# Kernel tuning notes

Measured on AMD Instinct MI355X. Metric: run time of the kernel, lower is better.

## Reference

```python
import jax, jax.numpy as jnp
import numpy as np

N, D1, D2, BW, B = 8, 1024, 1024, 3, 1024
D = D1 * D2
RES_DENOS = [3.0, 5.0, 17.0, 257.0, 65537.0]  # [2^2-1, 2^2+1, 2^4+1, 2^8+1, 2^16+1]
SPLIT_TEMP = 0.01


def ste_floor(x):
    # forward: floor, backward: identity (matches custom round autograd.Function)
    return x + jax.lax.stop_gradient(jnp.floor(x) - x)


def quantize_weights(U, thres_mean):
    beta, alpha = jnp.max(U), jnp.min(U)
    s = (beta - alpha) / RES_DENOS[0]
    vals_sum = s * ste_floor(U / s)  # level 0
    col = jnp.arange(D)[None, :]
    for idx in range(1, BW):
        s = s / RES_DENOS[idx]
        res_err = U - vals_sum                                   # [N, D]
        order = jnp.argsort(res_err, axis=0)                     # [N, D] int
        sorted_err = jnp.take_along_axis(res_err, order, axis=0) # [N, D]
        delta = sorted_err[1:] - sorted_err[:-1]                 # [N-1, D]
        delta = delta / jnp.max(delta)
        # differentiable split points, one per gap between sorted rows
        sp = jax.nn.sigmoid((jnp.mean(delta, axis=1) - jax.nn.sigmoid(thres_mean)[0]) / SPLIT_TEMP)  # [N-1]
        b = jnp.round(sp)                                        # hard 0/1 boundary (zero grad, like torch branch)
        gid = jnp.concatenate([jnp.zeros((1,), sp.dtype), jnp.cumsum(b)]).astype(jnp.int32)  # [N] group id per row
        counts = jax.ops.segment_sum(jnp.ones((N,), U.dtype), gid, num_segments=N)           # [N]
        sums = jax.ops.segment_sum(sorted_err, gid, num_segments=N)                          # [N, D]
        means = sums / jnp.maximum(counts, 1.0)[:, None]
        # grad_ factor: sp at boundary rows, (1-sp) at interior rows, 1 for the last row
        factors = jnp.where(b == 1.0, sp, 1.0 - sp)              # [N-1], in (0,1)
        logf = jnp.concatenate([jnp.log(factors), jnp.zeros((1,), sp.dtype)])  # [N]
        grad_g = jnp.exp(jax.ops.segment_sum(logf, gid, num_segments=N))       # [N] per-group product
        t = grad_g[gid][:, None] * means[gid]                    # [N, D] group value broadcast to member rows
        # scatter back through the sort permutation (== one-hot transfer matmul)
        grouped = jnp.zeros_like(U).at[order, col].set(t)
        vals_sum = vals_sum + s * ste_floor(grouped / s)
    return vals_sum


def setup_inputs() -> dict:
    key = jax.random.key(0)
    kx, ku = jax.random.split(key)
    x = jax.random.normal(kx, (B, N, D1), dtype=jnp.float32)
    # kaiming_normal_ on (N, D): std = sqrt(2 / fan_in) with fan_in = D
    U = jax.random.normal(ku, (N, D), dtype=jnp.float32) * np.sqrt(2.0 / D).astype(np.float32)
    thres_mean = jnp.array([-0.405], dtype=jnp.float32)
    return {"x": x, "U": U, "thres_mean": thres_mean}


def reference(x, U, thres_mean):
    w = quantize_weights(U, thres_mean).reshape(N, D1, D2)
    return jnp.einsum('bnd,ndl->bnl', x, w)
```

## Files before the change

kernel.cpp:

```cpp
#include <hip/hip_runtime.h>
#include <hip/hip_bf16.h>
#include <stdint.h>

#define DD (1 << 20)
#define NPART 4096

typedef float v4f __attribute__((ext_vector_type(4)));
typedef __bf16 bf16x8 __attribute__((ext_vector_type(8)));

struct Scalars {
  float s;
  int   uniform;
  int   done;
  float coef[8];
  float cnti[8];
  int   isend[8];
};

struct Partial {
  double g[7];
  double mx;
};

static __device__ __forceinline__ unsigned short f2bf(float v) {
  unsigned u = __float_as_uint(v);
  u += 0x7fffu + ((u >> 16) & 1u);
  return (unsigned short)(u >> 16);
}

__global__ void k_minmax_partial(const float4* __restrict__ U4, float2* __restrict__ part) {
  int tid = threadIdx.x, bid = blockIdx.x;
  float mn = 3.4e38f, mx = -3.4e38f;
#pragma unroll
  for (int j = 0; j < 8; ++j) {
    float4 v = U4[(size_t)(bid * 8 + j) * 256 + tid];
    mn = fminf(mn, fminf(fminf(v.x, v.y), fminf(v.z, v.w)));
    mx = fmaxf(mx, fmaxf(fmaxf(v.x, v.y), fmaxf(v.z, v.w)));
  }
#pragma unroll
  for (int off = 32; off; off >>= 1) {
    mn = fminf(mn, __shfl_down(mn, off, 64));
    mx = fmaxf(mx, __shfl_down(mx, off, 64));
  }
  __shared__ float2 w4[4];
  if ((tid & 63) == 0) w4[tid >> 6] = make_float2(mn, mx);
  __syncthreads();
  if (tid == 0) {
    for (int i = 1; i < 4; ++i) { mn = fminf(mn, w4[i].x); mx = fmaxf(mx, w4[i].y); }
    part[bid] = make_float2(mn, mx);
  }
}

__global__ void k_minmax_final(const float2* __restrict__ part, Scalars* sc0) {
  int tid = threadIdx.x;
  float mn = 3.4e38f, mx = -3.4e38f;
#pragma unroll
  for (int j = 0; j < 4; ++j) {
    float2 p = part[j * 256 + tid];
    mn = fminf(mn, p.x); mx = fmaxf(mx, p.y);
  }
#pragma unroll
  for (int off = 32; off; off >>= 1) {
    mn = fminf(mn, __shfl_down(mn, off, 64));
    mx = fmaxf(mx, __shfl_down(mx, off, 64));
  }
  __shared__ float2 w4[4];
  if ((tid & 63) == 0) w4[tid >> 6] = make_float2(mn, mx);
  __syncthreads();
  if (tid == 0) {
    for (int i = 1; i < 4; ++i) { mn = fminf(mn, w4[i].x); mx = fmaxf(mx, w4[i].y); }
    sc0->s = (mx - mn) / 3.0f;
  }
}

#define CE2(a, b)                                                        \
  { float ra = r[a], rb = r[b]; int oa = ord[a], ob = ord[b];            \
    bool sw = (ra > rb) || (ra == rb && oa > ob);                        \
    r[a] = sw ? rb : ra; r[b] = sw ? ra : rb;                            \
    ord[a] = sw ? ob : oa; ord[b] = sw ? oa : ob; }

#define SORTNET8                                                          \
  CE2(0,1) CE2(2,3) CE2(4,5) CE2(6,7)                                     \
  CE2(0,2) CE2(1,3) CE2(4,6) CE2(5,7)                                     \
  CE2(1,2) CE2(5,6)                                                       \
  CE2(0,4) CE2(1,5) CE2(2,6) CE2(3,7)                                     \
  CE2(2,4) CE2(3,5)                                                       \
  CE2(1,2) CE2(3,4) CE2(5,6)

#define CEV(a, b) { float ra = q[a], rb = q[b]; q[a] = fminf(ra, rb); q[b] = fmaxf(ra, rb); }
#define SORTNET8V                                                         \
  CEV(0,1) CEV(2,3) CEV(4,5) CEV(6,7)                                     \
  CEV(0,2) CEV(1,3) CEV(4,6) CEV(5,7)                                     \
  CEV(1,2) CEV(5,6)                                                       \
  CEV(0,4) CEV(1,5) CEV(2,6) CEV(3,7)                                     \
  CEV(2,4) CEV(3,5)                                                       \
  CEV(1,2) CEV(3,4) CEV(5,6)

static __device__ __forceinline__ void stats_block_reduce(float dl[7], float mx,
                                                          Partial* __restrict__ po) {
#pragma unroll
  for (int off = 32; off; off >>= 1) {
#pragma unroll
    for (int g = 0; g < 7; ++g) dl[g] += __shfl_down(dl[g], off, 64);
    mx = fmaxf(mx, __shfl_down(mx, off, 64));
  }
  __shared__ double wsum[4][7];
  __shared__ float wmax[4];
  int lane = threadIdx.x & 63, wv = threadIdx.x >> 6;
  if (lane == 0) {
#pragma unroll
    for (int g = 0; g < 7; ++g) wsum[wv][g] = (double)dl[g];
    wmax[wv] = mx;
  }
  __syncthreads();
  if (threadIdx.x == 0) {
#pragma unroll
    for (int g = 0; g < 7; ++g)
      po->g[g] = wsum[0][g] + wsum[1][g] + wsum[2][g] + wsum[3][g];
    po->mx = (double)fmaxf(fmaxf(wmax[0], wmax[1]), fmaxf(wmax[2], wmax[3]));
  }
}

__global__ void k_scalars2(const Partial* __restrict__ part, const Scalars* __restrict__ scin,
                           Scalars* __restrict__ scout, Scalars* __restrict__ scnext,
                           const float* __restrict__ thres, float deno, float deno_next,
                           int check_done) {
  if (check_done && scout->done) return;
  int t = threadIdx.x;
  double g[7] = {0, 0, 0, 0, 0, 0, 0};
  double mx = 0.0;
#pragma unroll
  for (int j = 0; j < NPART / 256; ++j) {
    const Partial& p = part[j * 256 + t];
#pragma unroll
    for (int i = 0; i < 7; ++i) g[i] += p.g[i];
    mx = fmax(mx, p.mx);
  }
#pragma unroll
  for (int off = 32; off; off >>= 1) {
#pragma unroll
    for (int i = 0; i < 7; ++i) g[i] += __shfl_down(g[i], off, 64);
    mx = fmax(mx, __shfl_down(mx, off, 64));
  }
  __shared__ double sg[4][8];
  int lane = t & 63, wv = t >> 6;
  if (lane == 0) {
#pragma unroll
    for (int i = 0; i < 7; ++i) sg[wv][i] = g[i];
    sg[wv][7] = mx;
  }
  __syncthreads();
  if (t != 0) return;
#pragma unroll
  for (int i = 0; i < 7; ++i) g[i] = sg[0][i] + sg[1][i] + sg[2][i] + sg[3][i];
  mx = fmax(fmax(sg[0][7], sg[1][7]), fmax(sg[2][7], sg[3][7]));

  float s = scin->s / deno;
  scout->s = s;
  float md = (float)mx;
  float sigT = 1.f / (1.f + expf(-thres[0]));
  float sp[7], bb[7];
  float zmax = -1e30f;
  for (int gg = 0; gg < 7; ++gg) {
    float mean = (float)(g[gg] / ((double)DD * (double)md));
    float z = (mean - sigT) / 0.01f;
    zmax = fmaxf(zmax, z);
    sp[gg] = 1.f / (1.f + expf(-z));
    bb[gg] = rintf(sp[gg]);
  }
  int gid[8]; gid[0] = 0;
  for (int i = 1; i < 8; ++i) gid[i] = gid[i - 1] + (int)bb[i - 1];
  float counts[8] = {0, 0, 0, 0, 0, 0, 0, 0};
  for (int i = 0; i < 8; ++i) counts[gid[i]] += 1.f;
  float lsum[8] = {0, 0, 0, 0, 0, 0, 0, 0};
  for (int i = 0; i < 7; ++i) {
    float f = (bb[i] == 1.f) ? sp[i] : (1.f - sp[i]);
    lsum[gid[i]] += logf(f);
  }
  float gradg[8];
  for (int gg = 0; gg < 8; ++gg) gradg[gg] = expf(lsum[gg]);
  for (int i = 0; i < 8; ++i) {
    scout->coef[i] = gradg[gid[i]];
    scout->cnti[i] = fmaxf(counts[gid[i]], 1.f);
    scout->isend[i] = (i == 7) || (gid[i + 1] != gid[i]);
  }
  int uni = (gid[7] == 0) ? 1 : 0;
  scout->uniform = uni;

  if (scnext) {
    if (uni && zmax < -21.0f) {
      scnext->s = s / deno_next;
      scnext->uniform = 1;
#pragma unroll
      for (int i = 0; i < 8; ++i) {
        scnext->coef[i] = 1.0f;
        scnext->cnti[i] = 8.0f;
        scnext->isend[i] = (i == 7) ? 1 : 0;
      }
      scnext->done = 1;
    } else {
      scnext->done = 0;
    }
  }
}

static __device__ __forceinline__ void update_core(const float u[8], const float vo[8],
                                                   const Scalars* __restrict__ sc,
                                                   float vnew[8]) {
  float s = sc->s;
  float coef[8], cnti[8]; int isend[8];
#pragma unroll
  for (int i = 0; i < 8; ++i) { coef[i] = sc->coef[i]; cnti[i] = sc->cnti[i]; isend[i] = sc->isend[i]; }
  float r[8]; int ord[8];
#pragma unroll
  for (int n = 0; n < 8; ++n) { r[n] = u[n] - vo[n]; ord[n] = n; }
  SORTNET8
  float endsum[8]; float a = 0.f;
#pragma unroll
  for (int i = 0; i < 8; ++i) { a += r[i]; endsum[i] = a; if (isend[i]) a = 0.f; }
  float t[8]; float gsv = 0.f;
#pragma unroll
  for (int i = 7; i >= 0; --i) {
    if (isend[i]) gsv = endsum[i];
    t[i] = coef[i] * (gsv / cnti[i]);
  }
#pragma unroll
  for (int n = 0; n < 8; ++n) {
    float tv = 0.f;
#pragma unroll
    for (int i = 0; i < 8; ++i) tv = (ord[i] == n) ? t[i] : tv;
    vnew[n] = vo[n] + s * floorf(tv / s);
  }
}

static __device__ __forceinline__ float uniform_delta(const float u[8], const float vo[8],
                                                      float coef0, float cnt0, float s) {
  float q[8];
#pragma unroll
  for (int n = 0; n < 8; ++n) q[n] = u[n] - vo[n];
  SORTNET8V
  float a = 0.f;
#pragma unroll
  for (int i = 0; i < 8; ++i) a += q[i];
  float t = coef0 * (a / cnt0);
  return s * floorf(t / s);
}

static __device__ __forceinline__ void apply_update(const float u[8], const float vo[8],
                                                    const Scalars* __restrict__ sc,
                                                    float vnew[8]) {
  if (sc->uniform) {
    float c = uniform_delta(u, vo, sc->coef[0], sc->cnti[0], sc->s);
#pragma unroll
    for (int n = 0; n < 8; ++n) vnew[n] = vo[n] + c;
  } else {
    update_core(u, vo, sc, vnew);
  }
}

__global__ void k_stats0(const float* __restrict__ U, Partial* __restrict__ part,
                         const Scalars* __restrict__ sc0,
                         const float* __restrict__ x, unsigned short* __restrict__ xT) {
  int t = threadIdx.x;
  if (blockIdx.x < NPART) {
    int d = blockIdx.x * 256 + t;
    float s = sc0->s;
    float q[8];
#pragma unroll
    for (int n = 0; n < 8; ++n) {
      float u = U[((size_t)n << 20) + d];
      q[n] = u - s * floorf(u / s);
    }
    SORTNET8V
    float dl[7]; float mx = 0.f;
#pragma unroll
    for (int g = 0; g < 7; ++g) { dl[g] = q[g + 1] - q[g]; mx = fmaxf(mx, dl[g]); }
    stats_block_reduce(dl, mx, &part[blockIdx.x]);
  } else {
    int bid2 = blockIdx.x - NPART;
#pragma unroll
    for (int j = 0; j < 4; ++j) {
      int i = j * (2048 * 256) + bid2 * 256 + t;
      int kq = i & 255;
      int b  = (i >> 8) & 1023;
      int n  = i >> 18;
      float4 v = *(const float4*)(x + ((size_t)(b * 8 + n) << 10) + (kq << 2));
      ushort4 o = make_ushort4(f2bf(v.x), f2bf(v.y), f2bf(v.z), f2bf(v.w));
      *(ushort4*)(xT + (((size_t)(n << 10 | b)) << 10) + (kq << 2)) = o;
    }
  }
}

__global__ void k_stats1(const float* __restrict__ U, Partial* __restrict__ part,
                         const Scalars* __restrict__ sc0, const Scalars* __restrict__ sc1,
                         const Scalars* __restrict__ sc2) {
  if (sc2->done) return;
  int d = blockIdx.x * 256 + threadIdx.x;
  float s0 = sc0->s;
  float u[8], v0[8], v1[8];
#pragma unroll
  for (int n = 0; n < 8; ++n) {
    u[n] = U[((size_t)n << 20) + d];
    v0[n] = s0 * floorf(u[n] / s0);
  }
  apply_update(u, v0, sc1, v1);
  float q[8];
#pragma unroll
  for (int n = 0; n < 8; ++n) q[n] = u[n] - v1[n];
  SORTNET8V
  float dl[7]; float mx = 0.f;
#pragma unroll
  for (int g = 0; g < 7; ++g) { dl[g] = q[g + 1] - q[g]; mx = fmaxf(mx, dl[g]); }
  stats_block_reduce(dl, mx, &part[blockIdx.x]);
}

__global__ void k_final_pack(const float* __restrict__ U,
                             const Scalars* __restrict__ sc0, const Scalars* __restrict__ sc1,
                             const Scalars* __restrict__ sc2, unsigned short* __restrict__ wT) {
  __shared__ unsigned short stile[8][32][34];
  int t = threadIdx.x;
  int k0 = (blockIdx.x >> 5) * 32;
  int l0 = (blockIdx.x & 31) * 32;
  float s0 = sc0->s;
  int kk = t >> 3;
  int lq = t & 7;
  int d0 = (k0 + kk) * 1024 + l0 + lq * 4;
  float4 u4[8];
#pragma unroll
  for (int n = 0; n < 8; ++n) u4[n] = *(const float4*)(U + ((size_t)n << 20) + d0);
#pragma unroll
  for (int j = 0; j < 4; ++j) {
    float u[8], v0[8], v1[8], v2[8];
#pragma unroll
    for (int n = 0; n < 8; ++n) {
      u[n] = ((const float*)&u4[n])[j];
      v0[n] = s0 * floorf(u[n] / s0);
    }
    apply_update(u, v0, sc1, v1);
    apply_update(u, v1, sc2, v2);
#pragma unroll
    for (int n = 0; n < 8; ++n) stile[n][kk][lq * 4 + j] = f2bf(v2[n]);
  }
  __syncthreads();
  int ll = t >> 3, kq = t & 7;
#pragma unroll
  for (int n = 0; n < 8; ++n) {
    ushort4 o;
    o.x = stile[n][kq * 4 + 0][ll];
    o.y = stile[n][kq * 4 + 1][ll];
    o.z = stile[n][kq * 4 + 2][ll];
    o.w = stile[n][kq * 4 + 3][ll];
    *(ushort4*)(wT + ((size_t)n << 20) + (size_t)(l0 + ll) * 1024 + k0 + kq * 4) = o;
  }
}

__global__ __launch_bounds__(256, 2)
void k_gemm(const unsigned short* __restrict__ xT, const unsigned short* __restrict__ wT,
            float* __restrict__ out) {
  __shared__ bf16x8 sA[1024];
  __shared__ bf16x8 sB[1024];
  const int n  = blockIdx.x;
  const int m0 = blockIdx.y * 128;
  const int l0 = blockIdx.z * 128;
  const int tid = threadIdx.x;
  const int lane = tid & 63;
  const int wv = tid >> 6;
  const int wm = (wv & 1) * 64;
  const int wl = (wv >> 1) * 64;
  const unsigned short* A  = xT + ((size_t)n << 20);
  const unsigned short* Bt = wT + ((size_t)n << 20);

  v4f acc[4][4] = {};
  const int quad = lane >> 4;
  const int r16 = lane & 15;

  for (int kt = 0; kt < 1024; kt += 64) {
#pragma unroll
    for (int rr = 0; rr < 4; ++rr) {
      int cb = rr * 4 + wv;
      int c = cb * 64 + lane;
      int row = c >> 3;
      int gc = (c & 7) ^ (row & 7);
      const unsigned short* ga = A  + (size_t)(m0 + row) * 1024 + kt + gc * 8;
      const unsigned short* gb = Bt + (size_t)(l0 + row) * 1024 + kt + gc * 8;
      __builtin_amdgcn_global_load_lds((const __attribute__((address_space(1))) void*)ga,
                                       (__attribute__((address_space(3))) void*)&sA[cb * 64],
                                       16, 0, 0);
      __builtin_amdgcn_global_load_lds((const __attribute__((address_space(1))) void*)gb,
                                       (__attribute__((address_space(3))) void*)&sB[cb * 64],
                                       16, 0, 0);
    }
    asm volatile("s_waitcnt vmcnt(0)" ::: "memory");
    __syncthreads();

#pragma unroll
    for (int ks = 0; ks < 2; ++ks) {
      bf16x8 af[4], bfr[4];
#pragma unroll
      for (int t = 0; t < 4; ++t) {
        int arow = wm + t * 16 + r16;
        af[t] = sA[arow * 8 + ((ks * 4 + quad) ^ (arow & 7))];
        int brow = wl + t * 16 + r16;
        bfr[t] = sB[brow * 8 + ((ks * 4 + quad) ^ (brow & 7))];
      }
#pragma unroll
      for (int tm = 0; tm < 4; ++tm)
#pragma unroll
        for (int tn = 0; tn < 4; ++tn)
          acc[tm][tn] = __builtin_amdgcn_mfma_f32_16x16x32_bf16(af[tm], bfr[tn], acc[tm][tn], 0, 0, 0);
    }
    __syncthreads();
  }

#pragma unroll
  for (int tm = 0; tm < 4; ++tm)
#pragma unroll
    for (int tn = 0; tn < 4; ++tn)
#pragma unroll
      for (int rr = 0; rr < 4; ++rr) {
        int row = m0 + wm + tm * 16 + quad * 4 + rr;
        int col = l0 + wl + tn * 16 + r16;
        out[(size_t)(row * 8 + n) * 1024 + col] = acc[tm][tn][rr];
      }
}

extern "C" void kernel_launch(void* const* d_in, const int* in_sizes, int n_in,
                              void* d_out, int out_size, void* d_ws, size_t ws_size,
                              hipStream_t stream) {
  const float* x = (const float*)d_in[0];
  const float* U = (const float*)d_in[1];
  const float* thres = (const float*)d_in[2];
  float* out = (float*)d_out;

  char* w = (char*)d_ws;
  Scalars* sc = (Scalars*)w;
  float2* mmpart = (float2*)(w + 4096);
  unsigned short* xT = (unsigned short*)(w + 16384);
  unsigned short* wT = xT + ((size_t)8 << 20);
  Partial* part = (Partial*)(w + 16384 + ((size_t)32 << 20));

  k_minmax_partial<<<1024, 256, 0, stream>>>((const float4*)U, mmpart);
  k_minmax_final<<<1, 256, 0, stream>>>(mmpart, &sc[0]);
  k_stats0<<<NPART + 2048, 256, 0, stream>>>(U, part, &sc[0], x, xT);
  k_scalars2<<<1, 256, 0, stream>>>(part, &sc[0], &sc[1], &sc[2], thres, 5.0f, 17.0f, 0);
  k_stats1<<<NPART, 256, 0, stream>>>(U, part, &sc[0], &sc[1], &sc[2]);
  k_scalars2<<<1, 256, 0, stream>>>(part, &sc[1], &sc[2], nullptr, thres, 17.0f, 0.0f, 1);
  k_final_pack<<<1024, 256, 0, stream>>>(U, &sc[0], &sc[1], &sc[2], wT);
  k_gemm<<<dim3(8, 8, 8), 256, 0, stream>>>(xT, wT, out);
}
```

Measured before the change: 165.8 us.

## Fold single-block scalar reductions into consumer kernels and cut launch count

Removes the separate minmax-final and two single-block scalar kernels. Each consumer block now recomputes the scale and the split-point scalars redundantly from the partials into shared memory. The minmax partial pass is merged with the x transpose/pack, and the stats kernels process four columns per thread, which cuts the partial count from 4096 to 1024. The goal is fewer launches and serial single-block gaps, paid for with redundant per-block reduction work over the partial arrays.

```diff
diff --git a/kernel.cpp b/kernel.cpp
--- a/kernel.cpp
+++ b/kernel.cpp
@@ -3,7 +3,6 @@
 #include <stdint.h>
 
 #define DD (1 << 20)
-#define NPART 4096
 
 typedef float v4f __attribute__((ext_vector_type(4)));
 typedef __bf16 bf16x8 __attribute__((ext_vector_type(8)));
@@ -11,7 +10,6 @@
 struct Scalars {
   float s;
   int   uniform;
-  int   done;
   float coef[8];
   float cnti[8];
   int   isend[8];
@@ -26,51 +24,6 @@
   unsigned u = __float_as_uint(v);
   u += 0x7fffu + ((u >> 16) & 1u);
   return (unsigned short)(u >> 16);
-}
-
-__global__ void k_minmax_partial(const float4* __restrict__ U4, float2* __restrict__ part) {
-  int tid = threadIdx.x, bid = blockIdx.x;
-  float mn = 3.4e38f, mx = -3.4e38f;
-#pragma unroll
-  for (int j = 0; j < 8; ++j) {
-    float4 v = U4[(size_t)(bid * 8 + j) * 256 + tid];
-    mn = fminf(mn, fminf(fminf(v.x, v.y), fminf(v.z, v.w)));
-    mx = fmaxf(mx, fmaxf(fmaxf(v.x, v.y), fmaxf(v.z, v.w)));
-  }
-#pragma unroll
-  for (int off = 32; off; off >>= 1) {
-    mn = fminf(mn, __shfl_down(mn, off, 64));
-    mx = fmaxf(mx, __shfl_down(mx, off, 64));
-  }
-  __shared__ float2 w4[4];
-  if ((tid & 63) == 0) w4[tid >> 6] = make_float2(mn, mx);
-  __syncthreads();
-  if (tid == 0) {
-    for (int i = 1; i < 4; ++i) { mn = fminf(mn, w4[i].x); mx = fmaxf(mx, w4[i].y); }
-    part[bid] = make_float2(mn, mx);
-  }
-}
-
-__global__ void k_minmax_final(const float2* __restrict__ part, Scalars* sc0) {
-  int tid = threadIdx.x;
-  float mn = 3.4e38f, mx = -3.4e38f;
-#pragma unroll
-  for (int j = 0; j < 4; ++j) {
-    float2 p = part[j * 256 + tid];
-    mn = fminf(mn, p.x); mx = fmaxf(mx, p.y);
-  }
-#pragma unroll
-  for (int off = 32; off; off >>= 1) {
-    mn = fminf(mn, __shfl_down(mn, off, 64));
-    mx = fmaxf(mx, __shfl_down(mx, off, 64));
-  }
-  __shared__ float2 w4[4];
-  if ((tid & 63) == 0) w4[tid >> 6] = make_float2(mn, mx);
-  __syncthreads();
-  if (tid == 0) {
-    for (int i = 1; i < 4; ++i) { mn = fminf(mn, w4[i].x); mx = fmaxf(mx, w4[i].y); }
-    sc0->s = (mx - mn) / 3.0f;
-  }
 }
 
 #define CE2(a, b)                                                        \
@@ -121,16 +74,42 @@
   }
 }
 
-__global__ void k_scalars2(const Partial* __restrict__ part, const Scalars* __restrict__ scin,
-                           Scalars* __restrict__ scout, Scalars* __restrict__ scnext,
-                           const float* __restrict__ thres, float deno, float deno_next,
-                           int check_done) {
-  if (check_done && scout->done) return;
+static __device__ __forceinline__ float compute_s0(const float2* __restrict__ mmpart) {
+  __shared__ float2 wmm[4];
+  __shared__ float sS0;
   int t = threadIdx.x;
-  double g[7] = {0, 0, 0, 0, 0, 0, 0};
-  double mx = 0.0;
-#pragma unroll
-  for (int j = 0; j < NPART / 256; ++j) {
+  float mn = 3.4e38f, mxv = -3.4e38f;
+#pragma unroll
+  for (int j = 0; j < 4; ++j) {
+    float2 p = mmpart[j * 256 + t];
+    mn = fminf(mn, p.x); mxv = fmaxf(mxv, p.y);
+  }
+#pragma unroll
+  for (int off = 32; off; off >>= 1) {
+    mn = fminf(mn, __shfl_down(mn, off, 64));
+    mxv = fmaxf(mxv, __shfl_down(mxv, off, 64));
+  }
+  int lane = t & 63, wv = t >> 6;
+  if (lane == 0) wmm[wv] = make_float2(mn, mxv);
+  __syncthreads();
+  if (t == 0) {
+    for (int i = 1; i < 4; ++i) { mn = fminf(mn, wmm[i].x); mxv = fmaxf(mxv, wmm[i].y); }
+    sS0 = (mxv - mn) / 3.0f;
+  }
+  __syncthreads();
+  return sS0;
+}
+
+static __device__ __forceinline__ void reduce_partials(const Partial* __restrict__ part,
+                                                       double g[7], double& mx) {
+  __shared__ double sg[4][8];
+  int t = threadIdx.x;
+  __syncthreads();
+#pragma unroll
+  for (int i = 0; i < 7; ++i) g[i] = 0.0;
+  mx = 0.0;
+#pragma unroll
+  for (int j = 0; j < 4; ++j) {
     const Partial& p = part[j * 256 + t];
 #pragma unroll
     for (int i = 0; i < 7; ++i) g[i] += p.g[i];
@@ -142,7 +121,6 @@
     for (int i = 0; i < 7; ++i) g[i] += __shfl_down(g[i], off, 64);
     mx = fmax(mx, __shfl_down(mx, off, 64));
   }
-  __shared__ double sg[4][8];
   int lane = t & 63, wv = t >> 6;
   if (lane == 0) {
 #pragma unroll
@@ -150,15 +128,19 @@
     sg[wv][7] = mx;
   }
   __syncthreads();
-  if (t != 0) return;
-#pragma unroll
-  for (int i = 0; i < 7; ++i) g[i] = sg[0][i] + sg[1][i] + sg[2][i] + sg[3][i];
-  mx = fmax(fmax(sg[0][7], sg[1][7]), fmax(sg[2][7], sg[3][7]));
-
-  float s = scin->s / deno;
-  scout->s = s;
+  if (t == 0) {
+#pragma unroll
+    for (int i = 0; i < 7; ++i) g[i] = sg[0][i] + sg[1][i] + sg[2][i] + sg[3][i];
+    mx = fmax(fmax(sg[0][7], sg[1][7]), fmax(sg[2][7], sg[3][7]));
+  }
+}
+
+static __device__ void make_scalars(const double g[7], double mx, float s_prev, float deno,
+                                    float thres0, Scalars* sc, bool* sat) {
+  float s = s_prev / deno;
+  sc->s = s;
   float md = (float)mx;
-  float sigT = 1.f / (1.f + expf(-thres[0]));
+  float sigT = 1.f / (1.f + expf(-thres0));
   float sp[7], bb[7];
   float zmax = -1e30f;
   for (int gg = 0; gg < 7; ++gg) {
@@ -180,28 +162,13 @@
   float gradg[8];
   for (int gg = 0; gg < 8; ++gg) gradg[gg] = expf(lsum[gg]);
   for (int i = 0; i < 8; ++i) {
-    scout->coef[i] = gradg[gid[i]];
-    scout->cnti[i] = fmaxf(counts[gid[i]], 1.f);
-    scout->isend[i] = (i == 7) || (gid[i + 1] != gid[i]);
+    sc->coef[i] = gradg[gid[i]];
+    sc->cnti[i] = fmaxf(counts[gid[i]], 1.f);
+    sc->isend[i] = (i == 7) || (gid[i + 1] != gid[i]);
   }
   int uni = (gid[7] == 0) ? 1 : 0;
-  scout->uniform = uni;
-
-  if (scnext) {
-    if (uni && zmax < -21.0f) {
-      scnext->s = s / deno_next;
-      scnext->uniform = 1;
-#pragma unroll
-      for (int i = 0; i < 8; ++i) {
-        scnext->coef[i] = 1.0f;
-        scnext->cnti[i] = 8.0f;
-        scnext->isend[i] = (i == 7) ? 1 : 0;
-      }
-      scnext->done = 1;
-    } else {
-      scnext->done = 0;
-    }
-  }
+  sc->uniform = uni;
+  *sat = (uni && zmax < -21.0f);
 }
 
 static __device__ __forceinline__ void update_core(const float u[8], const float vo[8],
@@ -258,29 +225,36 @@
   }
 }
 
-__global__ void k_stats0(const float* __restrict__ U, Partial* __restrict__ part,
-                         const Scalars* __restrict__ sc0,
-                         const float* __restrict__ x, unsigned short* __restrict__ xT) {
-  int t = threadIdx.x;
-  if (blockIdx.x < NPART) {
-    int d = blockIdx.x * 256 + t;
-    float s = sc0->s;
-    float q[8];
-#pragma unroll
-    for (int n = 0; n < 8; ++n) {
-      float u = U[((size_t)n << 20) + d];
-      q[n] = u - s * floorf(u / s);
-    }
-    SORTNET8V
-    float dl[7]; float mx = 0.f;
-#pragma unroll
-    for (int g = 0; g < 7; ++g) { dl[g] = q[g + 1] - q[g]; mx = fmaxf(mx, dl[g]); }
-    stats_block_reduce(dl, mx, &part[blockIdx.x]);
+__global__ __launch_bounds__(256)
+void k1_minmax_xpack(const float4* __restrict__ U4, float2* __restrict__ mmpart,
+                     const float* __restrict__ x, unsigned short* __restrict__ xT) {
+  int tid = threadIdx.x;
+  if (blockIdx.x < 1024) {
+    int bid = blockIdx.x;
+    float mn = 3.4e38f, mx = -3.4e38f;
+#pragma unroll
+    for (int j = 0; j < 8; ++j) {
+      float4 v = U4[(size_t)(bid * 8 + j) * 256 + tid];
+      mn = fminf(mn, fminf(fminf(v.x, v.y), fminf(v.z, v.w)));
+      mx = fmaxf(mx, fmaxf(fmaxf(v.x, v.y), fmaxf(v.z, v.w)));
+    }
+#pragma unroll
+    for (int off = 32; off; off >>= 1) {
+      mn = fminf(mn, __shfl_down(mn, off, 64));
+      mx = fmaxf(mx, __shfl_down(mx, off, 64));
+    }
+    __shared__ float2 w4[4];
+    if ((tid & 63) == 0) w4[tid >> 6] = make_float2(mn, mx);
+    __syncthreads();
+    if (tid == 0) {
+      for (int i = 1; i < 4; ++i) { mn = fminf(mn, w4[i].x); mx = fmaxf(mx, w4[i].y); }
+      mmpart[bid] = make_float2(mn, mx);
+    }
   } else {
-    int bid2 = blockIdx.x - NPART;
+    int bid2 = blockIdx.x - 1024;
 #pragma unroll
     for (int j = 0; j < 4; ++j) {
-      int i = j * (2048 * 256) + bid2 * 256 + t;
+      int i = j * (2048 * 256) + bid2 * 256 + tid;
       int kq = i & 255;
       int b  = (i >> 8) & 1023;
       int n  = i >> 18;
@@ -291,37 +265,115 @@
   }
 }
 
-__global__ void k_stats1(const float* __restrict__ U, Partial* __restrict__ part,
-                         const Scalars* __restrict__ sc0, const Scalars* __restrict__ sc1,
-                         const Scalars* __restrict__ sc2) {
-  if (sc2->done) return;
-  int d = blockIdx.x * 256 + threadIdx.x;
-  float s0 = sc0->s;
-  float u[8], v0[8], v1[8];
-#pragma unroll
-  for (int n = 0; n < 8; ++n) {
-    u[n] = U[((size_t)n << 20) + d];
-    v0[n] = s0 * floorf(u[n] / s0);
-  }
-  apply_update(u, v0, sc1, v1);
-  float q[8];
-#pragma unroll
-  for (int n = 0; n < 8; ++n) q[n] = u[n] - v1[n];
-  SORTNET8V
-  float dl[7]; float mx = 0.f;
-#pragma unroll
-  for (int g = 0; g < 7; ++g) { dl[g] = q[g + 1] - q[g]; mx = fmaxf(mx, dl[g]); }
-  stats_block_reduce(dl, mx, &part[blockIdx.x]);
-}
-
-__global__ void k_final_pack(const float* __restrict__ U,
-                             const Scalars* __restrict__ sc0, const Scalars* __restrict__ sc1,
-                             const Scalars* __restrict__ sc2, unsigned short* __restrict__ wT) {
+__global__ __launch_bounds__(256)
+void k2_stats0(const float* __restrict__ U, const float2* __restrict__ mmpart,
+               Partial* __restrict__ part) {
+  float s0 = compute_s0(mmpart);
+  int t = threadIdx.x;
+  size_t d0 = (size_t)blockIdx.x * 1024 + t * 4;
+  float4 u4[8];
+#pragma unroll
+  for (int n = 0; n < 8; ++n) u4[n] = *(const float4*)(U + ((size_t)n << 20) + d0);
+  float dl[7] = {0, 0, 0, 0, 0, 0, 0};
+  float mxv = 0.f;
+#pragma unroll
+  for (int j = 0; j < 4; ++j) {
+    float q[8];
+#pragma unroll
+    for (int n = 0; n < 8; ++n) {
+      float u = ((const float*)&u4[n])[j];
+      q[n] = u - s0 * floorf(u / s0);
+    }
+    SORTNET8V
+#pragma unroll
+    for (int g = 0; g < 7; ++g) { float dd = q[g + 1] - q[g]; dl[g] += dd; mxv = fmaxf(mxv, dd); }
+  }
+  stats_block_reduce(dl, mxv, &part[blockIdx.x]);
+}
+
+__global__ __launch_bounds__(256)
+void k3a_stats1(const float* __restrict__ U, const float2* __restrict__ mmpart,
+                const Partial* __restrict__ part, Partial* __restrict__ part2,
+                const float* __restrict__ thres) {
+  __shared__ Scalars ssc1;
+  __shared__ int ssat;
+  float s0 = compute_s0(mmpart);
+  double g[7]; double mx;
+  reduce_partials(part, g, mx);
+  if (threadIdx.x == 0) {
+    bool sat;
+    make_scalars(g, mx, s0, 5.0f, thres[0], &ssc1, &sat);
+    ssat = sat ? 1 : 0;
+  }
+  __syncthreads();
+  if (ssat) return;
+
+  int t = threadIdx.x;
+  size_t d0 = (size_t)blockIdx.x * 1024 + t * 4;
+  float4 u4[8];
+#pragma unroll
+  for (int n = 0; n < 8; ++n) u4[n] = *(const float4*)(U + ((size_t)n << 20) + d0);
+  float dl[7] = {0, 0, 0, 0, 0, 0, 0};
+  float mxv = 0.f;
+#pragma unroll
+  for (int j = 0; j < 4; ++j) {
+    float u[8], v0[8], v1[8];
+#pragma unroll
+    for (int n = 0; n < 8; ++n) {
+      u[n] = ((const float*)&u4[n])[j];
+      v0[n] = s0 * floorf(u[n] / s0);
+    }
+    apply_update(u, v0, &ssc1, v1);
+    float q[8];
+#pragma unroll
+    for (int n = 0; n < 8; ++n) q[n] = u[n] - v1[n];
+    SORTNET8V
+#pragma unroll
+    for (int gg = 0; gg < 7; ++gg) { float dd = q[gg + 1] - q[gg]; dl[gg] += dd; mxv = fmaxf(mxv, dd); }
+  }
+  stats_block_reduce(dl, mxv, &part2[blockIdx.x]);
+}
+
+__global__ __launch_bounds__(256)
+void k3b_final(const float* __restrict__ U, const float2* __restrict__ mmpart,
+               const Partial* __restrict__ part, const Partial* __restrict__ part2,
+               const float* __restrict__ thres, unsigned short* __restrict__ wT) {
+  __shared__ Scalars ssc1, ssc2;
+  __shared__ int ssat;
   __shared__ unsigned short stile[8][32][34];
   int t = threadIdx.x;
+  float s0 = compute_s0(mmpart);
+  {
+    double g[7]; double mx;
+    reduce_partials(part, g, mx);
+    if (t == 0) {
+      bool sat;
+      make_scalars(g, mx, s0, 5.0f, thres[0], &ssc1, &sat);
+      ssat = sat ? 1 : 0;
+    }
+  }
+  __syncthreads();
+  if (!ssat) {
+    double g[7]; double mx;
+    reduce_partials(part2, g, mx);
+    if (t == 0) {
+      bool sat2;
+      make_scalars(g, mx, ssc1.s, 17.0f, thres[0], &ssc2, &sat2);
+    }
+  } else if (t == 0) {
+    ssc2.s = ssc1.s / 17.0f;
+    ssc2.uniform = 1;
+#pragma unroll
+    for (int i = 0; i < 8; ++i) {
+      ssc2.coef[i] = 1.0f;
+      ssc2.cnti[i] = 8.0f;
+      ssc2.isend[i] = (i == 7) ? 1 : 0;
+    }
+  }
+  __syncthreads();
+
   int k0 = (blockIdx.x >> 5) * 32;
   int l0 = (blockIdx.x & 31) * 32;
-  float s0 = sc0->s;
   int kk = t >> 3;
   int lq = t & 7;
   int d0 = (k0 + kk) * 1024 + l0 + lq * 4;
@@ -336,8 +388,8 @@
       u[n] = ((const float*)&u4[n])[j];
       v0[n] = s0 * floorf(u[n] / s0);
     }
-    apply_update(u, v0, sc1, v1);
-    apply_update(u, v1, sc2, v2);
+    apply_update(u, v0, &ssc1, v1);
+    apply_update(u, v1, &ssc2, v2);
 #pragma unroll
     for (int n = 0; n < 8; ++n) stile[n][kk][lq * 4 + j] = f2bf(v2[n]);
   }
@@ -397,11 +449,11 @@
     for (int ks = 0; ks < 2; ++ks) {
       bf16x8 af[4], bfr[4];
 #pragma unroll
-      for (int t = 0; t < 4; ++t) {
-        int arow = wm + t * 16 + r16;
-        af[t] = sA[arow * 8 + ((ks * 4 + quad) ^ (arow & 7))];
-        int brow = wl + t * 16 + r16;
-        bfr[t] = sB[brow * 8 + ((ks * 4 + quad) ^ (brow & 7))];
+      for (int tt = 0; tt < 4; ++tt) {
+        int arow = wm + tt * 16 + r16;
+        af[tt] = sA[arow * 8 + ((ks * 4 + quad) ^ (arow & 7))];
+        int brow = wl + tt * 16 + r16;
+        bfr[tt] = sB[brow * 8 + ((ks * 4 + quad) ^ (brow & 7))];
       }
 #pragma unroll
       for (int tm = 0; tm < 4; ++tm)
@@ -433,18 +485,15 @@
   float* out = (float*)d_out;
 
   char* w = (char*)d_ws;
-  Scalars* sc = (Scalars*)w;
-  float2* mmpart = (float2*)(w + 4096);
-  unsigned short* xT = (unsigned short*)(w + 16384);
+  float2* mmpart = (float2*)w;
+  Partial* part  = (Partial*)(w + 8192);
+  Partial* part2 = (Partial*)(w + 8192 + 65536);
+  unsigned short* xT = (unsigned short*)(w + (1 << 20));
   unsigned short* wT = xT + ((size_t)8 << 20);
-  Partial* part = (Partial*)(w + 16384 + ((size_t)32 << 20));
-
-  k_minmax_partial<<<1024, 256, 0, stream>>>((const float4*)U, mmpart);
-  k_minmax_final<<<1, 256, 0, stream>>>(mmpart, &sc[0]);
-  k_stats0<<<NPART + 2048, 256, 0, stream>>>(U, part, &sc[0], x, xT);
-  k_scalars2<<<1, 256, 0, stream>>>(part, &sc[0], &sc[1], &sc[2], thres, 5.0f, 17.0f, 0);
-  k_stats1<<<NPART, 256, 0, stream>>>(U, part, &sc[0], &sc[1], &sc[2]);
-  k_scalars2<<<1, 256, 0, stream>>>(part, &sc[1], &sc[2], nullptr, thres, 17.0f, 0.0f, 1);
-  k_final_pack<<<1024, 256, 0, stream>>>(U, &sc[0], &sc[1], &sc[2], wT);
+
+  k1_minmax_xpack<<<3072, 256, 0, stream>>>((const float4*)U, mmpart, x, xT);
+  k2_stats0<<<1024, 256, 0, stream>>>(U, mmpart, part);
+  k3a_stats1<<<1024, 256, 0, stream>>>(U, mmpart, part, part2, thres);
+  k3b_final<<<1024, 256, 0, stream>>>(U, mmpart, part, part2, thres, wT);
   k_gemm<<<dim3(8, 8, 8), 256, 0, stream>>>(xT, wT, out);
 }
```

Measured after the change: 168.1 us. No clear change (+1.4%).
